# Performance work log

Hardware: AMD Instinct MI355X
Metric: run time of the kernel (lower is better)

The kernel has to match this reference:

```python
import jax, jax.numpy as jnp
import numpy as np

EPS = 1e-5

def conv1x1(x, w, b):
    # x: [B,C,H,W], w: [O,C], b: [O]
    return jnp.einsum('oc,bchw->bohw', w, x) + b[None, :, None, None]

def mean_variance_norm(feat):
    # per-(batch,channel) stats over spatial dims; torch.var default is unbiased (ddof=1)
    b, c = feat.shape[:2]
    flat = feat.reshape(b, c, -1)
    mean = jnp.mean(flat, axis=2)[:, :, None, None]
    std = jnp.sqrt(jnp.var(flat, axis=2, ddof=1) + EPS)[:, :, None, None]
    return (feat - mean) / std

def setup_inputs() -> dict:
    key = jax.random.key(0)
    ks = jax.random.split(key, 10)
    B, C, H, W = 4, 256, 64, 64
    sc = 1.0 / np.sqrt(C)
    return {
        'content': jax.random.normal(ks[0], (B, C, H, W), jnp.float32),
        'style': jax.random.normal(ks[1], (B, C, H, W), jnp.float32),
        'content_key': jax.random.normal(ks[2], (B, C, H, W), jnp.float32),
        'style_key': jax.random.normal(ks[3], (B, C, H, W), jnp.float32),
        'f_w': jax.random.normal(ks[4], (C, C), jnp.float32) * sc,
        'f_b': jax.random.normal(ks[5], (C,), jnp.float32) * 0.01,
        'g_w': jax.random.normal(ks[6], (C, C), jnp.float32) * sc,
        'g_b': jax.random.normal(ks[7], (C,), jnp.float32) * 0.01,
        'h_w': jax.random.normal(ks[8], (C, C), jnp.float32) * sc,
        'h_b': jax.random.normal(ks[9], (C,), jnp.float32) * 0.01,
    }

def reference(content, style, content_key, style_key, f_w, f_b, g_w, g_b, h_w, h_b):
    Fq = conv1x1(content_key, f_w, f_b)   # [B,C,Hc,Wc]
    G = conv1x1(style_key, g_w, g_b)      # [B,C,Hs,Ws]
    Hv = conv1x1(style, h_w, h_b)         # [B,C,Hs,Ws]
    b, c, h, w = Fq.shape
    hw_c = h * w
    hw_s = G.shape[2] * G.shape[3]
    Fm = Fq.reshape(b, c, hw_c).transpose(0, 2, 1)       # [B,Nq,C]
    Gm = G.reshape(b, c, hw_s)                            # [B,C,Nk]
    style_flat = Hv.reshape(b, c, hw_s).transpose(0, 2, 1)  # [B,Nk,C]
    S = jax.nn.softmax(jnp.einsum('bqc,bck->bqk', Fm, Gm), axis=-1)  # [B,Nq,Nk]
    mean = jnp.einsum('bqk,bkc->bqc', S, style_flat)
    second = jnp.einsum('bqk,bkc->bqc', S, style_flat ** 2)
    std = jnp.sqrt(jax.nn.relu(second - mean ** 2))
    mean = mean.reshape(b, h, w, c).transpose(0, 3, 1, 2)
    std = std.reshape(b, h, w, c).transpose(0, 3, 1, 2)
    return std * mean_variance_norm(content) + mean
```

## Files before the change

kernel.cpp:

```cpp
#include <hip/hip_runtime.h>
#include <math.h>

#define NSP 4096
#define CD  256
#define LOG2E 1.44269504f

typedef _Float16 half8 __attribute__((ext_vector_type(8)));
typedef _Float16 half4v __attribute__((ext_vector_type(4)));
typedef float f32x4 __attribute__((ext_vector_type(4)));
typedef unsigned int u32;

#define VMCNT(n) asm volatile("s_waitcnt vmcnt(" #n ")" ::: "memory")
#define LGKM0    asm volatile("s_waitcnt lgkmcnt(0)" ::: "memory")

__device__ __forceinline__ void gl16(const void* g, void* l) {
    __builtin_amdgcn_global_load_lds((const __attribute__((address_space(1))) u32*)g,
                                     (__attribute__((address_space(3))) u32*)l, 16, 0, 0);
}

template<int MODE>
__global__ __launch_bounds__(256, 2) void conv_kernel(
    const float* __restrict__ W, const float* __restrict__ bias,
    const float* __restrict__ Xall, _Float16* __restrict__ Yh, _Float16* __restrict__ Yl)
{
    const int b = blockIdx.z;
    const float* X = Xall + (size_t)b * CD * NSP;
    _Float16* Yhb = Yh + (size_t)b * CD * NSP * (MODE == 2 ? 2 : 1);
    _Float16* Ylb = (MODE == 2) ? nullptr : Yl + (size_t)b * CD * NSP;
    __shared__ float Ws[16][128];
    __shared__ float Xs[16][128];
    const int t = threadIdx.x;
    const int tx = t & 15, ty = t >> 4;
    const int m0 = blockIdx.y * 128, n0 = blockIdx.x * 128;
    float acc[8][8];
#pragma unroll
    for (int i = 0; i < 8; ++i)
#pragma unroll
        for (int j = 0; j < 8; ++j) acc[i][j] = 0.f;

    for (int k0 = 0; k0 < CD; k0 += 16) {
        __syncthreads();
        {
            int m = t >> 1, k = (t & 1) * 8;
            float4 w0 = *reinterpret_cast<const float4*>(&W[(size_t)(m0 + m) * CD + k0 + k]);
            float4 w1 = *reinterpret_cast<const float4*>(&W[(size_t)(m0 + m) * CD + k0 + k + 4]);
            Ws[k + 0][m] = w0.x; Ws[k + 1][m] = w0.y; Ws[k + 2][m] = w0.z; Ws[k + 3][m] = w0.w;
            Ws[k + 4][m] = w1.x; Ws[k + 5][m] = w1.y; Ws[k + 6][m] = w1.z; Ws[k + 7][m] = w1.w;
        }
        {
            int k = t >> 4, n = (t & 15) * 8;
            *reinterpret_cast<float4*>(&Xs[k][n]) =
                *reinterpret_cast<const float4*>(&X[(size_t)(k0 + k) * NSP + n0 + n]);
            *reinterpret_cast<float4*>(&Xs[k][n + 4]) =
                *reinterpret_cast<const float4*>(&X[(size_t)(k0 + k) * NSP + n0 + n + 4]);
        }
        __syncthreads();
#pragma unroll
        for (int k = 0; k < 16; ++k) {
            float a[8], bb[8];
            float4 a0 = *reinterpret_cast<const float4*>(&Ws[k][ty * 8]);
            float4 a1 = *reinterpret_cast<const float4*>(&Ws[k][ty * 8 + 4]);
            float4 b0 = *reinterpret_cast<const float4*>(&Xs[k][tx * 4]);
            float4 b1 = *reinterpret_cast<const float4*>(&Xs[k][64 + tx * 4]);
            a[0]=a0.x; a[1]=a0.y; a[2]=a0.z; a[3]=a0.w;
            a[4]=a1.x; a[5]=a1.y; a[6]=a1.z; a[7]=a1.w;
            bb[0]=b0.x; bb[1]=b0.y; bb[2]=b0.z; bb[3]=b0.w;
            bb[4]=b1.x; bb[5]=b1.y; bb[6]=b1.z; bb[7]=b1.w;
#pragma unroll
            for (int i = 0; i < 8; ++i)
#pragma unroll
                for (int j = 0; j < 8; ++j) acc[i][j] = fmaf(a[i], bb[j], acc[i][j]);
        }
    }
    float bv[8];
#pragma unroll
    for (int i = 0; i < 8; ++i) bv[i] = bias[m0 + ty * 8 + i];

    if (MODE == 0) {
#pragma unroll
        for (int jj = 0; jj < 8; ++jj) {
            int n = n0 + ((jj < 4) ? (tx * 4 + jj) : (64 + tx * 4 + (jj - 4)));
            half4v h0, h1, l0, l1;
#pragma unroll
            for (int i = 0; i < 4; ++i) {
                float y0 = (acc[i][jj] + bv[i]) * LOG2E;
                _Float16 hh0 = (_Float16)y0; h0[i] = hh0; l0[i] = (_Float16)(y0 - (float)hh0);
                float y1 = (acc[i + 4][jj] + bv[i + 4]) * LOG2E;
                _Float16 hh1 = (_Float16)y1; h1[i] = hh1; l1[i] = (_Float16)(y1 - (float)hh1);
            }
            size_t off = (size_t)n * CD + m0 + ty * 8;
            *reinterpret_cast<half4v*>(&Yhb[off])     = h0;
            *reinterpret_cast<half4v*>(&Yhb[off + 4]) = h1;
            *reinterpret_cast<half4v*>(&Ylb[off])     = l0;
            *reinterpret_cast<half4v*>(&Ylb[off + 4]) = l1;
        }
    } else if (MODE == 1) {
#pragma unroll
        for (int jj = 0; jj < 8; ++jj) {
            int n = n0 + ((jj < 4) ? (tx * 4 + jj) : (64 + tx * 4 + (jj - 4)));
            int tile = n >> 5, key = n & 31;
            int g = (m0 + ty * 8) >> 3;
            size_t base = (size_t)tile * 8192 + (size_t)key * 256
                        + ((((g * 16)) ^ ((key & 7) << 4)) >> 1);
            half4v h0, h1, l0, l1;
#pragma unroll
            for (int i = 0; i < 4; ++i) {
                float y0 = acc[i][jj] + bv[i];
                _Float16 hh0 = (_Float16)y0; h0[i] = hh0; l0[i] = (_Float16)(y0 - (float)hh0);
                float y1 = acc[i + 4][jj] + bv[i + 4];
                _Float16 hh1 = (_Float16)y1; h1[i] = hh1; l1[i] = (_Float16)(y1 - (float)hh1);
            }
            *reinterpret_cast<half4v*>(&Yhb[base])     = h0;
            *reinterpret_cast<half4v*>(&Yhb[base + 4]) = h1;
            *reinterpret_cast<half4v*>(&Ylb[base])     = l0;
            *reinterpret_cast<half4v*>(&Ylb[base + 4]) = l1;
        }
    } else {
#pragma unroll
        for (int i = 0; i < 8; ++i) {
            int ch = m0 + ty * 8 + i;
            int wv_ = ch >> 6, mv = (ch >> 4) & 3, lv = ch & 15;
            size_t chbase = (size_t)(wv_ * 8 + mv) * 512 + lv * 8;
#pragma unroll
            for (int grp = 0; grp < 2; ++grp) {
                int n = n0 + grp * 64 + tx * 4;
                int tile = n >> 5, kin = n & 31;
                int g4v = kin >> 3, pos0 = kin & 7;
                half4v hv, lv4;
#pragma unroll
                for (int j = 0; j < 4; ++j) {
                    float y = acc[i][grp * 4 + j] + bv[i];
                    _Float16 hh = (_Float16)y; hv[j] = hh; lv4[j] = (_Float16)(y - (float)hh);
                }
                size_t tb = (size_t)tile * 16384 + chbase + (size_t)g4v * 128 + pos0;
                *reinterpret_cast<half4v*>(&Yhb[tb])        = hv;
                *reinterpret_cast<half4v*>(&Yhb[tb + 2048]) = lv4;
            }
        }
    }
}

#define KB_OFF 0
#define PB_OFF 65536
#define RM_OFF 69632
#define SMEM_BYTES 69888

__global__ __launch_bounds__(256, 2) void attn_kernel(
    const _Float16* __restrict__ Qh_g, const _Float16* __restrict__ Ql_g,
    const _Float16* __restrict__ Kh_g, const _Float16* __restrict__ Kl_g,
    const _Float16* __restrict__ Vhl_g,
    float* __restrict__ Mout, float* __restrict__ Sout)
{
    extern __shared__ char smem[];
    const int tid = threadIdx.x;
    const int lane = tid & 63;
    const int w = tid >> 6;
    const int g4 = lane >> 4;
    const int l15 = lane & 15;
    const int kf = w & 1;
    const int qf = w >> 1;

    const int bid = blockIdx.x;
    const int b = (bid & 7) >> 1;
    const int qb = ((bid >> 3) << 1) | (bid & 1);
    const int q0 = qb * 32;

    const size_t bNC = (size_t)b * NSP * CD;
    const _Float16* Qhb = Qh_g + bNC;
    const _Float16* Qlb = Ql_g + bNC;
    const _Float16* Khb = Kh_g + bNC;
    const _Float16* Klb = Kl_g + bNC;
    const _Float16* Vb  = Vhl_g + bNC * 2;

    const int qrow = q0 + qf * 16 + l15;
    half8 qh[8], ql[8];
#pragma unroll
    for (int ks = 0; ks < 8; ++ks) {
        qh[ks] = *reinterpret_cast<const half8*>(Qhb + (size_t)qrow * CD + ks * 32 + g4 * 8);
        ql[ks] = *reinterpret_cast<const half8*>(Qlb + (size_t)qrow * CD + ks * 32 + g4 * 8);
    }

    auto stageK = [&](int t, int buf) {
        const _Float16* sh = Khb + (size_t)t * 8192 + tid * 8;
        const _Float16* sl = Klb + (size_t)t * 8192 + tid * 8;
        char* d = smem + KB_OFF + buf * 32768 + tid * 16;
#pragma unroll
        for (int j = 0; j < 4; ++j) {
            gl16(sh + j * 2048, d + j * 4096);
            gl16(sl + j * 2048, d + 16384 + j * 4096);
        }
    };

    stageK(0, 0); stageK(1, 1);

    f32x4 accM[4][2], accS[4][2];
#pragma unroll
    for (int m = 0; m < 4; ++m)
#pragma unroll
        for (int nf = 0; nf < 2; ++nf) {
            accM[m][nf] = (f32x4){0.f, 0.f, 0.f, 0.f};
            accS[m][nf] = (f32x4){0.f, 0.f, 0.f, 0.f};
        }
    float mrun = -3.0e38f, lrun = 0.f;

    half8 ones8;
#pragma unroll
    for (int e = 0; e < 8; ++e) ones8[e] = (_Float16)1.f;

    const int key = kf * 16 + l15;
    const int ksw = (key & 7) << 4;
    const int qloc = qf * 16 + l15;
    const int qsw = (qloc & 7) << 4;
    const size_t vlane = (size_t)g4 * 128 + (size_t)l15 * 8;

    half8 vh[4], vl[4];

    for (int t = 0; t < 128; ++t) {
        const int buf = t & 1;

        if (t <= 126) { VMCNT(8); } else { VMCNT(0); }
        LGKM0;
        __builtin_amdgcn_s_barrier();
        __builtin_amdgcn_sched_barrier(0);

        {
            const _Float16* Vt = Vb + (size_t)t * 16384;
#pragma unroll
            for (int m = 0; m < 4; ++m) {
                vh[m] = *reinterpret_cast<const half8*>(Vt + (size_t)(w * 8 + m) * 512 + vlane);
                vl[m] = *reinterpret_cast<const half8*>(Vt + (size_t)(w * 8 + 4 + m) * 512 + vlane);
            }
        }

        const char* krow = smem + KB_OFF + buf * 32768 + key * 512;
        f32x4 s = (f32x4){0.f, 0.f, 0.f, 0.f};
        __builtin_amdgcn_s_setprio(1);
#pragma unroll
        for (int ks = 0; ks < 8; ++ks) {
            int off = ((ks * 4 + g4) * 16) ^ ksw;
            half8 bh = *reinterpret_cast<const half8*>(krow + off);
            half8 bl = *reinterpret_cast<const half8*>(krow + 16384 + off);
            s = __builtin_amdgcn_mfma_f32_16x16x32_f16(bh, qh[ks], s, 0, 0, 0);
            s = __builtin_amdgcn_mfma_f32_16x16x32_f16(bh, ql[ks], s, 0, 0, 0);
            s = __builtin_amdgcn_mfma_f32_16x16x32_f16(bl, qh[ks], s, 0, 0, 0);
        }
        __builtin_amdgcn_s_setprio(0);

        float rmx = fmaxf(fmaxf(s[0], s[1]), fmaxf(s[2], s[3]));
        rmx = fmaxf(rmx, __shfl_xor(rmx, 16));
        rmx = fmaxf(rmx, __shfl_xor(rmx, 32));
        if (g4 == 0) ((float*)(smem + RM_OFF))[kf * 32 + l15 + qf * 16] = rmx;

        LGKM0;
        __builtin_amdgcn_s_barrier();
        __builtin_amdgcn_sched_barrier(0);

        if (t + 2 < 128) stageK(t + 2, buf);

        const float* rmf = (const float*)(smem + RM_OFF);
        int ql_ = lane & 31;
        float rm01 = fmaxf(rmf[ql_], rmf[32 + ql_]);
        bool upd = rm01 > mrun + 8.f;
        float sc = upd ? __builtin_amdgcn_exp2f(mrun - rm01) : 1.f;
        if (upd) mrun = rm01;

        float m_q = __shfl(mrun, qloc);
        half4v hp4;
#pragma unroll
        for (int e = 0; e < 4; ++e)
            hp4[e] = (_Float16)__builtin_amdgcn_exp2f(s[e] - m_q);
        *reinterpret_cast<half4v*>(smem + PB_OFF + qloc * 128 + ((kf * 32 + g4 * 8) ^ qsw)) = hp4;

        if (__ballot(sc < 1.f)) {
#pragma unroll
            for (int nf = 0; nf < 2; ++nf) {
                float scn = __shfl(sc, nf * 16 + l15);
#pragma unroll
                for (int m = 0; m < 4; ++m)
#pragma unroll
                    for (int e = 0; e < 4; ++e) { accM[m][nf][e] *= scn; accS[m][nf][e] *= scn; }
            }
        }

        LGKM0;
        __builtin_amdgcn_s_barrier();
        __builtin_amdgcn_sched_barrier(0);

        if (t <= 125) { VMCNT(8); } else { VMCNT(0); }

        half8 pb[2];
#pragma unroll
        for (int nf = 0; nf < 2; ++nf) {
            int q = nf * 16 + l15;
            pb[nf] = *reinterpret_cast<const half8*>(smem + PB_OFF + q * 128 + ((g4 * 16) ^ ((q & 7) << 4)));
        }
        f32x4 po[2];
#pragma unroll
        for (int nf = 0; nf < 2; ++nf) po[nf] = (f32x4){0.f, 0.f, 0.f, 0.f};
        __builtin_amdgcn_s_setprio(1);
#pragma unroll
        for (int nf = 0; nf < 2; ++nf)
            po[nf] = __builtin_amdgcn_mfma_f32_16x16x32_f16(ones8, pb[nf], po[nf], 0, 0, 0);
#pragma unroll
        for (int m = 0; m < 4; ++m) {
            half8 vh8 = vh[m], vl8 = vl[m];
            half8 wh8, wl8;
#pragma unroll
            for (int e = 0; e < 8; ++e) {
                float v = (float)vh8[e] + (float)vl8[e];
                float wv = v * v;
                _Float16 hh = (_Float16)wv;
                wh8[e] = hh; wl8[e] = (_Float16)(wv - (float)hh);
            }
#pragma unroll
            for (int nf = 0; nf < 2; ++nf) {
                accM[m][nf] = __builtin_amdgcn_mfma_f32_16x16x32_f16(vh8, pb[nf], accM[m][nf], 0, 0, 0);
                accM[m][nf] = __builtin_amdgcn_mfma_f32_16x16x32_f16(vl8, pb[nf], accM[m][nf], 0, 0, 0);
                accS[m][nf] = __builtin_amdgcn_mfma_f32_16x16x32_f16(wh8, pb[nf], accS[m][nf], 0, 0, 0);
                accS[m][nf] = __builtin_amdgcn_mfma_f32_16x16x32_f16(wl8, pb[nf], accS[m][nf], 0, 0, 0);
            }
        }
        __builtin_amdgcn_s_setprio(0);

        float rsum = (g4 & 1) ? po[1][0] : po[0][0];
        lrun = lrun * sc + rsum;
        __builtin_amdgcn_sched_barrier(0);
    }

    float inv = 1.f / lrun;
    float linv[2];
#pragma unroll
    for (int nf = 0; nf < 2; ++nf) linv[nf] = __shfl(inv, nf * 16 + l15);

#pragma unroll
    for (int m = 0; m < 4; ++m)
#pragma unroll
        for (int nf = 0; nf < 2; ++nf) {
            int qg = q0 + nf * 16 + l15;
#pragma unroll
            for (int e = 0; e < 4; ++e) {
                int ch = w * 64 + m * 16 + g4 * 4 + e;
                float mean = accM[m][nf][e] * linv[nf];
                float sec  = accS[m][nf][e] * linv[nf];
                float var = sec - mean * mean;
                float sd = sqrtf(fmaxf(var, 0.f));
                size_t off = ((size_t)b * CD + ch) * NSP + qg;
                Mout[off] = mean;
                Sout[off] = sd;
            }
        }
}

__global__ __launch_bounds__(256) void mvn_kernel(
    const float* __restrict__ content, const float* __restrict__ Mn,
    const float* __restrict__ Sd, float* __restrict__ out)
{
    __shared__ float redS[4], redSS[4];
    const int t = threadIdx.x;
    const size_t base = (size_t)blockIdx.x * NSP;
    const float4* x4 = reinterpret_cast<const float4*>(content + base);
    float s = 0.f, ss = 0.f;
    float4 xv[4];
#pragma unroll
    for (int i = 0; i < 4; ++i) {
        float4 v = x4[i * 256 + t];
        xv[i] = v;
        s  += v.x + v.y + v.z + v.w;
        ss += v.x * v.x + v.y * v.y + v.z * v.z + v.w * v.w;
    }
#pragma unroll
    for (int mk = 1; mk < 64; mk <<= 1) { s += __shfl_xor(s, mk); ss += __shfl_xor(ss, mk); }
    if ((t & 63) == 0) { redS[t >> 6] = s; redSS[t >> 6] = ss; }
    __syncthreads();
    float tot   = redS[0] + redS[1] + redS[2] + redS[3];
    float totss = redSS[0] + redSS[1] + redSS[2] + redSS[3];
    float mu  = tot * (1.f / 4096.f);
    float var = (totss - 4096.f * mu * mu) * (1.f / 4095.f);
    float rstd = 1.f / sqrtf(var + 1e-5f);
    const float4* m4 = reinterpret_cast<const float4*>(Mn + base);
    const float4* s4 = reinterpret_cast<const float4*>(Sd + base);
    float4* o4 = reinterpret_cast<float4*>(out + base);
#pragma unroll
    for (int i = 0; i < 4; ++i) {
        float4 mv = m4[i * 256 + t];
        float4 sv = s4[i * 256 + t];
        float4 v  = xv[i];
        float4 o;
        o.x = sv.x * ((v.x - mu) * rstd) + mv.x;
        o.y = sv.y * ((v.y - mu) * rstd) + mv.y;
        o.z = sv.z * ((v.z - mu) * rstd) + mv.z;
        o.w = sv.w * ((v.w - mu) * rstd) + mv.w;
        o4[i * 256 + t] = o;
    }
}

extern "C" void kernel_launch(void* const* d_in, const int* in_sizes, int n_in,
                              void* d_out, int out_size, void* d_ws, size_t ws_size,
                              hipStream_t stream)
{
    const float* content     = (const float*)d_in[0];
    const float* style       = (const float*)d_in[1];
    const float* content_key = (const float*)d_in[2];
    const float* style_key   = (const float*)d_in[3];
    const float* f_w = (const float*)d_in[4];
    const float* f_b = (const float*)d_in[5];
    const float* g_w = (const float*)d_in[6];
    const float* g_b = (const float*)d_in[7];
    const float* h_w = (const float*)d_in[8];
    const float* h_b = (const float*)d_in[9];
    float* out = (float*)d_out;

    const size_t TS = (size_t)4 * NSP * CD;
    _Float16* ws16 = (_Float16*)d_ws;
    _Float16* Qh  = ws16;
    _Float16* Ql  = ws16 + TS;
    _Float16* Kh  = ws16 + 2 * TS;
    _Float16* Kl  = ws16 + 3 * TS;
    _Float16* Vhl = ws16 + 4 * TS;
    float* Mn = (float*)(ws16 + 6 * TS);
    float* Sd = Mn + TS;

    dim3 cgrid(32, 2, 4);
    conv_kernel<0><<<cgrid, 256, 0, stream>>>(f_w, f_b, content_key, Qh, Ql);
    conv_kernel<1><<<cgrid, 256, 0, stream>>>(g_w, g_b, style_key, Kh, Kl);
    conv_kernel<2><<<cgrid, 256, 0, stream>>>(h_w, h_b, style, Vhl, Vhl);
    attn_kernel<<<dim3(512), 256, SMEM_BYTES, stream>>>(Qh, Ql, Kh, Kl, Vhl, Mn, Sd);
    mvn_kernel<<<dim3(1024), 256, 0, stream>>>(content, Mn, Sd, out);
}
```

Measured before the change: 566.0 us.

## Precompute V squared in conv, split QK accumulators, store mean/std as fp16

The V conv kernel now also writes the hi/lo fp16 split of V squared, so the attention loop no longer computes the squares and their splits on every tile. V loads move after the row-max barrier. The QK MFMA chain is split across three independent accumulators to break the dependency, and the PV MFMAs are regrouped by operand. Mean and std intermediates are stored as fp16, which halves that traffic into mvn_kernel but loses some precision, while V traffic in the attention loop doubles.

```diff
diff --git a/kernel.cpp b/kernel.cpp
--- a/kernel.cpp
+++ b/kernel.cpp
@@ -25,7 +25,7 @@
 {
     const int b = blockIdx.z;
     const float* X = Xall + (size_t)b * CD * NSP;
-    _Float16* Yhb = Yh + (size_t)b * CD * NSP * (MODE == 2 ? 2 : 1);
+    _Float16* Yhb = Yh + (size_t)b * CD * NSP * (MODE == 2 ? 4 : 1);
     _Float16* Ylb = (MODE == 2) ? nullptr : Yl + (size_t)b * CD * NSP;
     __shared__ float Ws[16][128];
     __shared__ float Xs[16][128];
@@ -120,21 +120,25 @@
         for (int i = 0; i < 8; ++i) {
             int ch = m0 + ty * 8 + i;
             int wv_ = ch >> 6, mv = (ch >> 4) & 3, lv = ch & 15;
-            size_t chbase = (size_t)(wv_ * 8 + mv) * 512 + lv * 8;
+            size_t chbase = (size_t)(wv_ * 16 + mv) * 512 + lv * 8;
 #pragma unroll
             for (int grp = 0; grp < 2; ++grp) {
                 int n = n0 + grp * 64 + tx * 4;
                 int tile = n >> 5, kin = n & 31;
                 int g4v = kin >> 3, pos0 = kin & 7;
-                half4v hv, lv4;
+                half4v hv, lv4, whv, wlv;
 #pragma unroll
                 for (int j = 0; j < 4; ++j) {
                     float y = acc[i][grp * 4 + j] + bv[i];
                     _Float16 hh = (_Float16)y; hv[j] = hh; lv4[j] = (_Float16)(y - (float)hh);
+                    float wy = y * y;
+                    _Float16 wh_ = (_Float16)wy; whv[j] = wh_; wlv[j] = (_Float16)(wy - (float)wh_);
                 }
-                size_t tb = (size_t)tile * 16384 + chbase + (size_t)g4v * 128 + pos0;
+                size_t tb = (size_t)tile * 32768 + chbase + (size_t)g4v * 128 + pos0;
                 *reinterpret_cast<half4v*>(&Yhb[tb])        = hv;
                 *reinterpret_cast<half4v*>(&Yhb[tb + 2048]) = lv4;
+                *reinterpret_cast<half4v*>(&Yhb[tb + 4096]) = whv;
+                *reinterpret_cast<half4v*>(&Yhb[tb + 6144]) = wlv;
             }
         }
     }
@@ -148,8 +152,8 @@
 __global__ __launch_bounds__(256, 2) void attn_kernel(
     const _Float16* __restrict__ Qh_g, const _Float16* __restrict__ Ql_g,
     const _Float16* __restrict__ Kh_g, const _Float16* __restrict__ Kl_g,
-    const _Float16* __restrict__ Vhl_g,
-    float* __restrict__ Mout, float* __restrict__ Sout)
+    const _Float16* __restrict__ Vq_g,
+    _Float16* __restrict__ Mout, _Float16* __restrict__ Sout)
 {
     extern __shared__ char smem[];
     const int tid = threadIdx.x;
@@ -170,7 +174,7 @@
     const _Float16* Qlb = Ql_g + bNC;
     const _Float16* Khb = Kh_g + bNC;
     const _Float16* Klb = Kl_g + bNC;
-    const _Float16* Vb  = Vhl_g + bNC * 2;
+    const _Float16* Vb  = Vq_g + bNC * 4;
 
     const int qrow = q0 + qf * 16 + l15;
     half8 qh[8], ql[8];
@@ -213,7 +217,7 @@
     const int qsw = (qloc & 7) << 4;
     const size_t vlane = (size_t)g4 * 128 + (size_t)l15 * 8;
 
-    half8 vh[4], vl[4];
+    half8 vh[4], vl[4], wh[4], wl[4];
 
     for (int t = 0; t < 128; ++t) {
         const int buf = t & 1;
@@ -223,28 +227,21 @@
         __builtin_amdgcn_s_barrier();
         __builtin_amdgcn_sched_barrier(0);
 
-        {
-            const _Float16* Vt = Vb + (size_t)t * 16384;
-#pragma unroll
-            for (int m = 0; m < 4; ++m) {
-                vh[m] = *reinterpret_cast<const half8*>(Vt + (size_t)(w * 8 + m) * 512 + vlane);
-                vl[m] = *reinterpret_cast<const half8*>(Vt + (size_t)(w * 8 + 4 + m) * 512 + vlane);
-            }
-        }
-
         const char* krow = smem + KB_OFF + buf * 32768 + key * 512;
-        f32x4 s = (f32x4){0.f, 0.f, 0.f, 0.f};
+        f32x4 sA = (f32x4){0.f, 0.f, 0.f, 0.f};
+        f32x4 sB = sA, sC = sA;
         __builtin_amdgcn_s_setprio(1);
 #pragma unroll
         for (int ks = 0; ks < 8; ++ks) {
             int off = ((ks * 4 + g4) * 16) ^ ksw;
             half8 bh = *reinterpret_cast<const half8*>(krow + off);
             half8 bl = *reinterpret_cast<const half8*>(krow + 16384 + off);
-            s = __builtin_amdgcn_mfma_f32_16x16x32_f16(bh, qh[ks], s, 0, 0, 0);
-            s = __builtin_amdgcn_mfma_f32_16x16x32_f16(bh, ql[ks], s, 0, 0, 0);
-            s = __builtin_amdgcn_mfma_f32_16x16x32_f16(bl, qh[ks], s, 0, 0, 0);
+            sA = __builtin_amdgcn_mfma_f32_16x16x32_f16(bh, qh[ks], sA, 0, 0, 0);
+            sB = __builtin_amdgcn_mfma_f32_16x16x32_f16(bh, ql[ks], sB, 0, 0, 0);
+            sC = __builtin_amdgcn_mfma_f32_16x16x32_f16(bl, qh[ks], sC, 0, 0, 0);
         }
         __builtin_amdgcn_s_setprio(0);
+        f32x4 s = (sA + sB) + sC;
 
         float rmx = fmaxf(fmaxf(s[0], s[1]), fmaxf(s[2], s[3]));
         rmx = fmaxf(rmx, __shfl_xor(rmx, 16));
@@ -255,6 +252,16 @@
         __builtin_amdgcn_s_barrier();
         __builtin_amdgcn_sched_barrier(0);
 
+        {
+            const _Float16* Vt = Vb + (size_t)t * 32768;
+#pragma unroll
+            for (int m = 0; m < 4; ++m) {
+                vh[m] = *reinterpret_cast<const half8*>(Vt + (size_t)(w * 16 + m) * 512 + vlane);
+                vl[m] = *reinterpret_cast<const half8*>(Vt + (size_t)(w * 16 + 4 + m) * 512 + vlane);
+                wh[m] = *reinterpret_cast<const half8*>(Vt + (size_t)(w * 16 + 8 + m) * 512 + vlane);
+                wl[m] = *reinterpret_cast<const half8*>(Vt + (size_t)(w * 16 + 12 + m) * 512 + vlane);
+            }
+        }
         if (t + 2 < 128) stageK(t + 2, buf);
 
         const float* rmf = (const float*)(smem + RM_OFF);
@@ -302,24 +309,25 @@
         for (int nf = 0; nf < 2; ++nf)
             po[nf] = __builtin_amdgcn_mfma_f32_16x16x32_f16(ones8, pb[nf], po[nf], 0, 0, 0);
 #pragma unroll
-        for (int m = 0; m < 4; ++m) {
-            half8 vh8 = vh[m], vl8 = vl[m];
-            half8 wh8, wl8;
-#pragma unroll
-            for (int e = 0; e < 8; ++e) {
-                float v = (float)vh8[e] + (float)vl8[e];
-                float wv = v * v;
-                _Float16 hh = (_Float16)wv;
-                wh8[e] = hh; wl8[e] = (_Float16)(wv - (float)hh);
-            }
-#pragma unroll
-            for (int nf = 0; nf < 2; ++nf) {
-                accM[m][nf] = __builtin_amdgcn_mfma_f32_16x16x32_f16(vh8, pb[nf], accM[m][nf], 0, 0, 0);
-                accM[m][nf] = __builtin_amdgcn_mfma_f32_16x16x32_f16(vl8, pb[nf], accM[m][nf], 0, 0, 0);
-                accS[m][nf] = __builtin_amdgcn_mfma_f32_16x16x32_f16(wh8, pb[nf], accS[m][nf], 0, 0, 0);
-                accS[m][nf] = __builtin_amdgcn_mfma_f32_16x16x32_f16(wl8, pb[nf], accS[m][nf], 0, 0, 0);
-            }
-        }
+        for (int m = 0; m < 4; ++m)
+#pragma unroll
+            for (int nf = 0; nf < 2; ++nf)
+                accM[m][nf] = __builtin_amdgcn_mfma_f32_16x16x32_f16(vh[m], pb[nf], accM[m][nf], 0, 0, 0);
+#pragma unroll
+        for (int m = 0; m < 4; ++m)
+#pragma unroll
+            for (int nf = 0; nf < 2; ++nf)
+                accM[m][nf] = __builtin_amdgcn_mfma_f32_16x16x32_f16(vl[m], pb[nf], accM[m][nf], 0, 0, 0);
+#pragma unroll
+        for (int m = 0; m < 4; ++m)
+#pragma unroll
+            for (int nf = 0; nf < 2; ++nf)
+                accS[m][nf] = __builtin_amdgcn_mfma_f32_16x16x32_f16(wh[m], pb[nf], accS[m][nf], 0, 0, 0);
+#pragma unroll
+        for (int m = 0; m < 4; ++m)
+#pragma unroll
+            for (int nf = 0; nf < 2; ++nf)
+                accS[m][nf] = __builtin_amdgcn_mfma_f32_16x16x32_f16(wl[m], pb[nf], accS[m][nf], 0, 0, 0);
         __builtin_amdgcn_s_setprio(0);
 
         float rsum = (g4 & 1) ? po[1][0] : po[0][0];
@@ -345,15 +353,15 @@
                 float var = sec - mean * mean;
                 float sd = sqrtf(fmaxf(var, 0.f));
                 size_t off = ((size_t)b * CD + ch) * NSP + qg;
-                Mout[off] = mean;
-                Sout[off] = sd;
+                Mout[off] = (_Float16)mean;
+                Sout[off] = (_Float16)sd;
             }
         }
 }
 
 __global__ __launch_bounds__(256) void mvn_kernel(
-    const float* __restrict__ content, const float* __restrict__ Mn,
-    const float* __restrict__ Sd, float* __restrict__ out)
+    const float* __restrict__ content, const _Float16* __restrict__ Mn,
+    const _Float16* __restrict__ Sd, float* __restrict__ out)
 {
     __shared__ float redS[4], redSS[4];
     const int t = threadIdx.x;
@@ -377,19 +385,19 @@
     float mu  = tot * (1.f / 4096.f);
     float var = (totss - 4096.f * mu * mu) * (1.f / 4095.f);
     float rstd = 1.f / sqrtf(var + 1e-5f);
-    const float4* m4 = reinterpret_cast<const float4*>(Mn + base);
-    const float4* s4 = reinterpret_cast<const float4*>(Sd + base);
+    const half4v* m4 = reinterpret_cast<const half4v*>(Mn + base);
+    const half4v* s4 = reinterpret_cast<const half4v*>(Sd + base);
     float4* o4 = reinterpret_cast<float4*>(out + base);
 #pragma unroll
     for (int i = 0; i < 4; ++i) {
-        float4 mv = m4[i * 256 + t];
-        float4 sv = s4[i * 256 + t];
+        half4v mv = m4[i * 256 + t];
+        half4v sv = s4[i * 256 + t];
         float4 v  = xv[i];
         float4 o;
-        o.x = sv.x * ((v.x - mu) * rstd) + mv.x;
-        o.y = sv.y * ((v.y - mu) * rstd) + mv.y;
-        o.z = sv.z * ((v.z - mu) * rstd) + mv.z;
-        o.w = sv.w * ((v.w - mu) * rstd) + mv.w;
+        o.x = (float)sv[0] * ((v.x - mu) * rstd) + (float)mv[0];
+        o.y = (float)sv[1] * ((v.y - mu) * rstd) + (float)mv[1];
+        o.z = (float)sv[2] * ((v.z - mu) * rstd) + (float)mv[2];
+        o.w = (float)sv[3] * ((v.w - mu) * rstd) + (float)mv[3];
         o4[i * 256 + t] = o;
     }
 }
@@ -412,18 +420,18 @@
 
     const size_t TS = (size_t)4 * NSP * CD;
     _Float16* ws16 = (_Float16*)d_ws;
-    _Float16* Qh  = ws16;
-    _Float16* Ql  = ws16 + TS;
-    _Float16* Kh  = ws16 + 2 * TS;
-    _Float16* Kl  = ws16 + 3 * TS;
-    _Float16* Vhl = ws16 + 4 * TS;
-    float* Mn = (float*)(ws16 + 6 * TS);
-    float* Sd = Mn + TS;
+    _Float16* Qh = ws16;
+    _Float16* Ql = ws16 + TS;
+    _Float16* Kh = ws16 + 2 * TS;
+    _Float16* Kl = ws16 + 3 * TS;
+    _Float16* Vq = ws16 + 4 * TS;
+    _Float16* Mn = ws16 + 8 * TS;
+    _Float16* Sd = ws16 + 9 * TS;
 
     dim3 cgrid(32, 2, 4);
     conv_kernel<0><<<cgrid, 256, 0, stream>>>(f_w, f_b, content_key, Qh, Ql);
     conv_kernel<1><<<cgrid, 256, 0, stream>>>(g_w, g_b, style_key, Kh, Kl);
-    conv_kernel<2><<<cgrid, 256, 0, stream>>>(h_w, h_b, style, Vhl, Vhl);
-    attn_kernel<<<dim3(512), 256, SMEM_BYTES, stream>>>(Qh, Ql, Kh, Kl, Vhl, Mn, Sd);
+    conv_kernel<2><<<cgrid, 256, 0, stream>>>(h_w, h_b, style, Vq, Vq);
+    attn_kernel<<<dim3(512), 256, SMEM_BYTES, stream>>>(Qh, Ql, Kh, Kl, Vq, Mn, Sd);
     mvn_kernel<<<dim3(1024), 256, 0, stream>>>(content, Mn, Sd, out);
 }
```

New measurement: 549.3 us. 1.03x faster.
